# Kernel tuning notes

Hardware: AMD Instinct MI355X
Metric: run time of the kernel (lower is better)

The kernel has to match this reference:

```python
import jax, jax.numpy as jnp
import numpy as np
from jax import lax

_SHARPEN = jnp.array([[-1., -1., -1.], [-1., 9., -1.], [-1., -1., -1.]], dtype=jnp.float32)


def setup_inputs() -> dict:
    key = jax.random.key(0)
    k1, k2, k3, k4, k5 = jax.random.split(key, 5)
    B, C, H, W = 32, 3, 512, 512
    x = jax.random.uniform(k1, (B, C, H, W), dtype=jnp.float32)
    gamma = 0.5 + jax.random.uniform(k2, (B,), dtype=jnp.float32)            # [0.5, 1.5)
    wb = 0.8 + 0.4 * jax.random.uniform(k3, (B, 3), dtype=jnp.float32)       # [0.8, 1.2)
    contrast = 0.8 + 0.4 * jax.random.uniform(k4, (B,), dtype=jnp.float32)   # [0.8, 1.2)
    sharpen_strength = jax.random.uniform(k5, (B,), dtype=jnp.float32)       # [0, 1)
    return {"x": x, "gamma": gamma, "wb": wb, "contrast": contrast,
            "sharpen_strength": sharpen_strength}


def reference(x, gamma, wb, contrast, sharpen_strength):
    B, C, H, W = x.shape
    g = gamma[:, None, None, None]
    x = x ** g                                       # tone curve
    x = x * wb[:, :, None, None]                     # white balance
    mean = jnp.mean(x, axis=(2, 3), keepdims=True)   # per-channel mean
    x = jnp.clip((x - mean) * contrast[:, None, None, None] + mean, 0.0, 1.0)
    # depthwise 3x3 sharpen (same kernel per channel)
    kern = jnp.tile(_SHARPEN.astype(x.dtype)[None, None], (C, 1, 1, 1))  # [C,1,3,3]
    x_sharp = lax.conv_general_dilated(
        x, kern, window_strides=(1, 1), padding=((1, 1), (1, 1)),
        dimension_numbers=("NCHW", "OIHW", "NCHW"), feature_group_count=C)
    s = sharpen_strength[:, None, None, None]
    return jnp.clip(x_sharp * s + x * (1.0 - s), 0.0, 1.0)
```

## Files before the change

### kernel.cpp

```cpp
#include <hip/hip_runtime.h>


#define HH 512
#define WW 512
#define NPLANE (HH * WW)
#define NPLANES 96
#define CHUNKS 8

typedef float f4 __attribute__((ext_vector_type(4)));

__device__ __forceinline__ float fpow(float v, float g) {
    return __builtin_amdgcn_exp2f(g * __builtin_amdgcn_logf(v));
}
__device__ __forceinline__ float tfm(float v, float g, float wbc, float mean, float ct) {
    float p = fpow(v, g) * wbc;
    return __saturatef((p - mean) * ct + mean);
}

__global__ __launch_bounds__(256) void mean_kernel(
    const float* __restrict__ x,
    const float* __restrict__ gamma,
    float* __restrict__ partials)
{
    const int blk   = blockIdx.x;
    const int plane = blk / CHUNKS;
    const float g   = gamma[plane / 3];

    const float4* xp = (const float4*)(x + (size_t)plane * NPLANE)
                       + (size_t)(blk % CHUNKS) * (NPLANE / CHUNKS / 4);
    const int tid = threadIdx.x;

    float acc = 0.f;
    #pragma unroll
    for (int i = 0; i < 32; ++i) {
        float4 v = xp[i * 256 + tid];
        acc += fpow(v.x, g) + fpow(v.y, g) + fpow(v.z, g) + fpow(v.w, g);
    }
    #pragma unroll
    for (int off = 32; off > 0; off >>= 1)
        acc += __shfl_down(acc, off, 64);

    __shared__ float wsum[4];
    if ((tid & 63) == 0) wsum[tid >> 6] = acc;
    __syncthreads();
    if (tid == 0) partials[blk] = wsum[0] + wsum[1] + wsum[2] + wsum[3];
}

#define TR 16
#define LSTRIDE 520

__global__ __launch_bounds__(256, 4) void fuse_kernel(
    const float* __restrict__ x,
    const float* __restrict__ gamma,
    const float* __restrict__ wb,
    const float* __restrict__ contrast,
    const float* __restrict__ sharpen,
    const float* __restrict__ partials,
    float* __restrict__ out)
{
    __shared__ float tile[(TR + 2) * LSTRIDE];

    const int plane = blockIdx.y;
    const int tileY = blockIdx.x;
    const int b     = plane / 3;
    const float g   = gamma[b];
    const float wbc = wb[plane];
    const float ct  = contrast[b];
    const float s   = sharpen[b];

    float psum = 0.f;
    const float* pp = partials + plane * CHUNKS;
    #pragma unroll
    for (int i = 0; i < CHUNKS; ++i) psum += pp[i];
    const float mean = psum * wbc * (1.0f / (float)NPLANE);

    const float* xp = x + (size_t)plane * NPLANE;
    const int y0  = tileY * TR;
    const int tid = threadIdx.x;

    #pragma unroll
    for (int ii = 0; ii < 9; ++ii) {
        int i  = ii * 256 + tid;
        int r  = i >> 7;
        int c4 = i & 127;
        int gy = y0 - 1 + r;
        float4* dst = (float4*)&tile[r * LSTRIDE + 4 + c4 * 4];
        if (gy < 0 || gy >= HH) {
            *dst = make_float4(0.f, 0.f, 0.f, 0.f);
        } else {
            float4 v = ((const float4*)(xp + (size_t)gy * WW))[c4];
            *dst = make_float4(tfm(v.x, g, wbc, mean, ct),
                               tfm(v.y, g, wbc, mean, ct),
                               tfm(v.z, g, wbc, mean, ct),
                               tfm(v.w, g, wbc, mean, ct));
        }
    }
    if (tid < TR + 2) {
        tile[tid * LSTRIDE + 3]   = 0.f;
        tile[tid * LSTRIDE + 516] = 0.f;
    }
    __syncthreads();

    float* op = out + (size_t)plane * NPLANE;
    const float c1 = 1.0f + 9.0f * s;

    const int lane = tid & 63;
    const int wave = tid >> 6;
    const int cg   = wave & 1;
    const int rg   = wave >> 1;
    const int c0   = cg * 256 + lane * 4;
    const int jb   = rg * 8;

    auto ldrow = [&](int r, f4& h, f4& m) {
        const float* p = &tile[r * LSTRIDE + c0];
        f4 A = *(const f4*)(p);
        f4 B = *(const f4*)(p + 4);
        f4 C = *(const f4*)(p + 8);
        h.x = A.w + B.x + B.y;
        h.y = B.x + B.y + B.z;
        h.z = B.y + B.z + B.w;
        h.w = B.z + B.w + C.x;
        m = B;
    };

    f4 h0, h1, h2, m1, m2, mdum;
    ldrow(jb,     h0, mdum);
    ldrow(jb + 1, h1, m1);

    #pragma unroll 4
    for (int j = 0; j < 8; ++j) {
        ldrow(jb + 2 + j, h2, m2);
        f4 sum = h0 + h1 + h2;
        f4 o;
        o.x = __saturatef(fmaf(c1, m1.x, -s * sum.x));
        o.y = __saturatef(fmaf(c1, m1.y, -s * sum.y));
        o.z = __saturatef(fmaf(c1, m1.z, -s * sum.z));
        o.w = __saturatef(fmaf(c1, m1.w, -s * sum.w));
        __builtin_nontemporal_store(o, (f4*)(op + (size_t)(y0 + jb + j) * WW + c0));
        h0 = h1; h1 = h2; m1 = m2;
    }
}

extern "C" void kernel_launch(void* const* d_in, const int* in_sizes, int n_in,
                              void* d_out, int out_size, void* d_ws, size_t ws_size,
                              hipStream_t stream) {
    const float* x        = (const float*)d_in[0];
    const float* gamma    = (const float*)d_in[1];
    const float* wb       = (const float*)d_in[2];
    const float* contrast = (const float*)d_in[3];
    const float* sharpen  = (const float*)d_in[4];
    float* out      = (float*)d_out;
    float* partials = (float*)d_ws;

    mean_kernel<<<dim3(NPLANES * CHUNKS), 256, 0, stream>>>(x, gamma, partials);
    fuse_kernel<<<dim3(32, NPLANES), 256, 0, stream>>>(x, gamma, wb, contrast,
                                                       sharpen, partials, out);
}
```

Measured before the change: 199.2 us.

## Replace LDS tile in sharpen kernel with per-wave register sliding window and shuffles

The fused transform+sharpen kernel no longer stages a transformed tile in shared memory. Each wave now owns a 256-column by 16-row strip. It streams rows through registers with one-row prefetch and gets horizontal neighbours from lane shuffles, with scalar loads for the strip edges. This removes the LDS traffic and the block barrier. In exchange the halo rows are recomputed per strip, including the pow transform, and the edge lanes issue extra uncoalesced scalar loads.

```diff
diff --git a/kernel.cpp b/kernel.cpp
--- a/kernel.cpp
+++ b/kernel.cpp
@@ -6,6 +6,7 @@
 #define NPLANE (HH * WW)
 #define NPLANES 96
 #define CHUNKS 8
+#define ROWS 16
 
 typedef float f4 __attribute__((ext_vector_type(4)));
 
@@ -46,10 +47,7 @@
     if (tid == 0) partials[blk] = wsum[0] + wsum[1] + wsum[2] + wsum[3];
 }
 
-#define TR 16
-#define LSTRIDE 520
-
-__global__ __launch_bounds__(256, 4) void fuse_kernel(
+__global__ __launch_bounds__(256) void fuse_kernel(
     const float* __restrict__ x,
     const float* __restrict__ gamma,
     const float* __restrict__ wb,
@@ -58,10 +56,15 @@
     const float* __restrict__ partials,
     float* __restrict__ out)
 {
-    __shared__ float tile[(TR + 2) * LSTRIDE];
+    const int tid  = threadIdx.x;
+    const int lane = tid & 63;
+    const int wave = tid >> 6;
+    const int wg   = blockIdx.x * 4 + wave;
+    const int plane = wg >> 6;
+    const int s6    = wg & 63;
+    const int base  = (s6 & 1) * 256;
+    const int y0    = (s6 >> 1) * ROWS;
 
-    const int plane = blockIdx.y;
-    const int tileY = blockIdx.x;
     const int b     = plane / 3;
     const float g   = gamma[b];
     const float wbc = wb[plane];
@@ -75,69 +78,60 @@
     const float mean = psum * wbc * (1.0f / (float)NPLANE);
 
     const float* xp = x + (size_t)plane * NPLANE;
-    const int y0  = tileY * TR;
-    const int tid = threadIdx.x;
+    float* op       = out + (size_t)plane * NPLANE;
+    const int ci    = (base >> 2) + lane;
+    const float c1  = 1.0f + 9.0f * s;
+
+    f4 hm2, hm1, mprev, vcur;
+    {
+        int r0 = y0 - 1;
+        vcur = (r0 >= 0) ? ((const f4*)(xp + (size_t)r0 * WW))[ci] : (f4)0.f;
+    }
 
     #pragma unroll
-    for (int ii = 0; ii < 9; ++ii) {
-        int i  = ii * 256 + tid;
-        int r  = i >> 7;
-        int c4 = i & 127;
-        int gy = y0 - 1 + r;
-        float4* dst = (float4*)&tile[r * LSTRIDE + 4 + c4 * 4];
-        if (gy < 0 || gy >= HH) {
-            *dst = make_float4(0.f, 0.f, 0.f, 0.f);
+    for (int idx = 0; idx < ROWS + 2; ++idx) {
+        const int r  = y0 - 1 + idx;
+        const int rn = r + 1;
+        f4 vnext = (f4)0.f;
+        if (idx < ROWS + 1 && rn < HH)
+            vnext = ((const f4*)(xp + (size_t)rn * WW))[ci];
+
+        f4 B;
+        const bool rv = (r >= 0) & (r < HH);
+        if (rv) {
+            B.x = tfm(vcur.x, g, wbc, mean, ct);
+            B.y = tfm(vcur.y, g, wbc, mean, ct);
+            B.z = tfm(vcur.z, g, wbc, mean, ct);
+            B.w = tfm(vcur.w, g, wbc, mean, ct);
         } else {
-            float4 v = ((const float4*)(xp + (size_t)gy * WW))[c4];
-            *dst = make_float4(tfm(v.x, g, wbc, mean, ct),
-                               tfm(v.y, g, wbc, mean, ct),
-                               tfm(v.z, g, wbc, mean, ct),
-                               tfm(v.w, g, wbc, mean, ct));
+            B = (f4)0.f;
         }
-    }
-    if (tid < TR + 2) {
-        tile[tid * LSTRIDE + 3]   = 0.f;
-        tile[tid * LSTRIDE + 516] = 0.f;
-    }
-    __syncthreads();
 
-    float* op = out + (size_t)plane * NPLANE;
-    const float c1 = 1.0f + 9.0f * s;
+        float eL = 0.f, eR = 0.f;
+        if (rv && lane == 0 && base > 0)
+            eL = tfm(xp[(size_t)r * WW + base - 1], g, wbc, mean, ct);
+        if (rv && lane == 63 && base + 256 < WW)
+            eR = tfm(xp[(size_t)r * WW + base + 256], g, wbc, mean, ct);
 
-    const int lane = tid & 63;
-    const int wave = tid >> 6;
-    const int cg   = wave & 1;
-    const int rg   = wave >> 1;
-    const int c0   = cg * 256 + lane * 4;
-    const int jb   = rg * 8;
+        float lo = __shfl_up(B.w, 1);  if (lane == 0)  lo = eL;
+        float hi = __shfl_down(B.x, 1); if (lane == 63) hi = eR;
 
-    auto ldrow = [&](int r, f4& h, f4& m) {
-        const float* p = &tile[r * LSTRIDE + c0];
-        f4 A = *(const f4*)(p);
-        f4 B = *(const f4*)(p + 4);
-        f4 C = *(const f4*)(p + 8);
-        h.x = A.w + B.x + B.y;
-        h.y = B.x + B.y + B.z;
-        h.z = B.y + B.z + B.w;
-        h.w = B.z + B.w + C.x;
-        m = B;
-    };
+        f4 hr;
+        hr.x = lo  + B.x + B.y;
+        hr.y = B.x + B.y + B.z;
+        hr.z = B.y + B.z + B.w;
+        hr.w = B.z + B.w + hi;
 
-    f4 h0, h1, h2, m1, m2, mdum;
-    ldrow(jb,     h0, mdum);
-    ldrow(jb + 1, h1, m1);
-
-    #pragma unroll 4
-    for (int j = 0; j < 8; ++j) {
-        ldrow(jb + 2 + j, h2, m2);
-        f4 sum = h0 + h1 + h2;
-        f4 o;
-        o.x = __saturatef(fmaf(c1, m1.x, -s * sum.x));
-        o.y = __saturatef(fmaf(c1, m1.y, -s * sum.y));
-        o.z = __saturatef(fmaf(c1, m1.z, -s * sum.z));
-        o.w = __saturatef(fmaf(c1, m1.w, -s * sum.w));
-        __builtin_nontemporal_store(o, (f4*)(op + (size_t)(y0 + jb + j) * WW + c0));
-        h0 = h1; h1 = h2; m1 = m2;
+        if (idx >= 2) {
+            f4 sum = hm2 + hm1 + hr;
+            f4 o;
+            o.x = __saturatef(fmaf(c1, mprev.x, -s * sum.x));
+            o.y = __saturatef(fmaf(c1, mprev.y, -s * sum.y));
+            o.z = __saturatef(fmaf(c1, mprev.z, -s * sum.z));
+            o.w = __saturatef(fmaf(c1, mprev.w, -s * sum.w));
+            __builtin_nontemporal_store(o, (f4*)(op + (size_t)(r - 1) * WW) + ci);
+        }
+        hm2 = hm1; hm1 = hr; mprev = B; vcur = vnext;
     }
 }
 
@@ -153,6 +147,6 @@
     float* partials = (float*)d_ws;
 
     mean_kernel<<<dim3(NPLANES * CHUNKS), 256, 0, stream>>>(x, gamma, partials);
-    fuse_kernel<<<dim3(32, NPLANES), 256, 0, stream>>>(x, gamma, wb, contrast,
-                                                       sharpen, partials, out);
+    fuse_kernel<<<dim3(6144 / 4), 256, 0, stream>>>(x, gamma, wb, contrast,
+                                                    sharpen, partials, out);
 }
```

Result: no change. 199.5 us (+0.2%).
